# Performance work log

Hardware: AMD Instinct MI355X
Metric: run time of the kernel (lower is better)

## Reference

```python
import jax, jax.numpy as jnp
import numpy as np

SEQ, BATCH, IN = 512, 64, 1024
H, L = 512, 2


def setup_inputs() -> dict:
    key = jax.random.key(0)
    ks = jax.random.split(key, 5)
    s = 0.02
    return {
        "x": jax.random.normal(ks[0], (SEQ, BATCH, IN), dtype=jnp.float32),
        "W_ih": jax.random.normal(ks[1], (L, 2, 4 * H, IN), dtype=jnp.float32) * s,
        "b_ih": jax.random.normal(ks[2], (L, 2, 4 * H), dtype=jnp.float32) * s,
        "W_hh": jax.random.normal(ks[3], (L, 2, 4 * H, H), dtype=jnp.float32) * s,
        "b_hh": jax.random.normal(ks[4], (L, 2, 4 * H), dtype=jnp.float32) * s,
    }


def _run_direction(xs, Wi, bi, Wh, bh, hidden):
    # Precompute the input projection for all timesteps in one big GEMM.
    pre = jnp.einsum("tbd,gd->tbg", xs, Wi) + bi  # [T, B, 4H]

    def step(carry, p):
        h, c = carry
        gates = p + h @ Wh.T + bh
        i, f, g, o = jnp.split(gates, 4, axis=-1)
        # NOTE: faithful to the source module's (nonstandard) gating:
        #   c_t = c_{t-1} * sigmoid(i) + sigmoid(f) * tanh(g)
        c = c * jax.nn.sigmoid(i) + jax.nn.sigmoid(f) * jnp.tanh(g)
        h = jnp.tanh(c) * jax.nn.sigmoid(o)
        return (h, c), h

    B = xs.shape[1]
    h0 = jnp.zeros((B, hidden), xs.dtype)
    c0 = jnp.zeros((B, hidden), xs.dtype)
    _, hs = jax.lax.scan(step, (h0, c0), pre)
    return hs  # [T, B, H]


def reference(x, W_ih, b_ih, W_hh, b_hh):
    hidden = W_hh.shape[-1]
    num_layers = W_ih.shape[0]
    inp = x  # [T, B, D]
    for l in range(num_layers):
        fwd = _run_direction(inp, W_ih[l, 0], b_ih[l, 0], W_hh[l, 0], b_hh[l, 0], hidden)
        bwd = _run_direction(inp[::-1], W_ih[l, 1], b_ih[l, 1], W_hh[l, 1], b_hh[l, 1], hidden)[::-1]
        inp = jnp.concatenate([fwd, bwd], axis=-1)  # [T, B, 2H]
    return inp
```

## Files before the change

kernel.cpp:

```cpp
#include <hip/hip_runtime.h>

#define TSEQ 512
#define BATCH 64
#define DIN 1024
#define HID 512
#define G4 2048
#define CHK 64

typedef __attribute__((ext_vector_type(8))) short short8;
typedef __attribute__((ext_vector_type(4))) float floatx4;

__device__ __forceinline__ floatx4 mfma16(short8 a, short8 b, floatx4 c) {
  return __builtin_amdgcn_mfma_f32_16x16x32_bf16(a, b, c, 0, 0, 0);
}

__device__ __forceinline__ unsigned short f2bf(float f) {
  unsigned int u = __float_as_uint(f);
  unsigned int r = (u + 0x7fffu + ((u >> 16) & 1u)) >> 16;
  return (unsigned short)r;
}

__device__ __forceinline__ float sigm(float x) { return 1.f / (1.f + __expf(-x)); }
__device__ __forceinline__ float tanh_f(float x) {
  float xx = fminf(fmaxf(x, -15.f), 15.f);
  float e = __expf(2.f * xx);
  return (e - 1.f) / (e + 1.f);
}

__device__ __forceinline__ unsigned long long coh_load_q(const unsigned long long* p) {
  return __hip_atomic_load(p, __ATOMIC_RELAXED, __HIP_MEMORY_SCOPE_AGENT);
}
__device__ __forceinline__ void coh_store_u32(unsigned int* p, unsigned int v) {
  __hip_atomic_store(p, v, __ATOMIC_RELAXED, __HIP_MEMORY_SCOPE_AGENT);
}

__global__ void k_convert_x(const float* __restrict__ x, unsigned short* __restrict__ xbf, int n4) {
  int i = blockIdx.x * 256 + threadIdx.x;
  if (i >= n4) return;
  floatx4 v = reinterpret_cast<const floatx4*>(x)[i];
  union { unsigned short us[4]; unsigned long long ull; } pk;
  pk.us[0] = f2bf(v[0]); pk.us[1] = f2bf(v[1]); pk.us[2] = f2bf(v[2]); pk.us[3] = f2bf(v[3]);
  reinterpret_cast<unsigned long long*>(xbf)[i] = pk.ull;
}

__global__ void k_prep_w(const float* __restrict__ W, unsigned short* __restrict__ Wf, int K) {
  int mt = blockIdx.x, kt = blockIdx.y, ld = blockIdx.z;
  int lane = threadIdx.x;
  int i = lane & 15;
  int unit = (mt >> 1) * 8 + (i >> 2) * 2 + (mt & 1);
  int row = (i & 3) * HID + unit;
  int k0 = kt * 32 + (lane >> 4) * 8;
  const float* src = W + (size_t)ld * G4 * K + (size_t)row * K + k0;
  unsigned short* dst = Wf + (size_t)ld * G4 * K + (((size_t)mt * (K / 32) + kt) * 64 + lane) * 8;
  for (int j = 0; j < 8; ++j) dst[j] = f2bf(src[j]);
}

__global__ void k_prep_bias(const float* __restrict__ bih, const float* __restrict__ bhh,
                            float* __restrict__ biasf) {
  int idx = blockIdx.x * 256 + threadIdx.x;
  int ld = idx >> 11;
  int rp = idx & 2047;
  int unit = (rp >> 5) * 8 + ((rp >> 2) & 3) * 2 + ((rp >> 4) & 1);
  int row = (rp & 3) * HID + unit;
  biasf[idx] = bih[ld * G4 + row] + bhh[ld * G4 + row];
}

__global__ void k_zero_bar(unsigned int* bar) {
  if (threadIdx.x < 2) bar[threadIdx.x * 64] = 0;
}

__global__ __launch_bounds__(256, 2) void k_proj(
    const unsigned short* __restrict__ xin,
    const unsigned short* __restrict__ Wf,
    const float* __restrict__ biasf,
    float* __restrict__ pre,
    int t0) {
  const int dir = blockIdx.z;
  const int w = threadIdx.x >> 6;
  const int lane = threadIdx.x & 63;
  const int quad = lane >> 4, col = lane & 15;
  const int tloc = blockIdx.y * 4 + w;
  const int tg = dir ? (TSEQ - 1 - (t0 + tloc)) : (t0 + tloc);
  const unsigned short* Wd = Wf + (size_t)dir * G4 * DIN;
  const unsigned short* xrow = xin + (size_t)tg * BATCH * DIN;

  floatx4 acc[8][4];
#pragma unroll
  for (int mi = 0; mi < 8; ++mi)
#pragma unroll
    for (int ni = 0; ni < 4; ++ni) acc[mi][ni] = (floatx4){0.f, 0.f, 0.f, 0.f};

#pragma unroll 4
  for (int kt = 0; kt < 32; ++kt) {
    short8 bfr[4];
#pragma unroll
    for (int ni = 0; ni < 4; ++ni) {
      int b = ni * 16 + col;
      bfr[ni] = *reinterpret_cast<const short8*>(xrow + (size_t)b * DIN + kt * 32 + quad * 8);
    }
#pragma unroll
    for (int mi = 0; mi < 8; ++mi) {
      size_t mt = (size_t)(blockIdx.x * 8 + mi);
      short8 afr = *reinterpret_cast<const short8*>(Wd + ((mt * 32 + kt) * 64 + lane) * 8);
#pragma unroll
      for (int ni = 0; ni < 4; ++ni) acc[mi][ni] = mfma16(afr, bfr[ni], acc[mi][ni]);
    }
  }

#pragma unroll
  for (int mi = 0; mi < 8; ++mi) {
    int gbase = blockIdx.x * 128 + mi * 16 + quad * 4;
#pragma unroll
    for (int r = 0; r < 4; ++r) {
      float bv = biasf[dir * G4 + gbase + r];
      float* prow = pre + (((size_t)dir * CHK + tloc) * G4 + gbase + r) * BATCH;
#pragma unroll
      for (int ni = 0; ni < 4; ++ni) prow[ni * 16 + col] = acc[mi][ni][r] + bv;
    }
  }
}

__device__ __forceinline__ void dir_barrier(unsigned int* ctr, unsigned int target) {
  __syncthreads();
  if (threadIdx.x == 0) {
    __hip_atomic_fetch_add(ctr, 1u, __ATOMIC_RELAXED, __HIP_MEMORY_SCOPE_AGENT);
    while (__hip_atomic_load(ctr, __ATOMIC_RELAXED, __HIP_MEMORY_SCOPE_AGENT) < target) {
      __builtin_amdgcn_s_sleep(1);
    }
  }
  __syncthreads();
}

__global__ __launch_bounds__(256, 1) void k_steps(
    const unsigned short* __restrict__ Whhf,
    const float* __restrict__ pre,
    unsigned short* act1bf,
    unsigned short* hT2,
    float* cst,
    float* __restrict__ dout,
    unsigned int* bar,
    int t0, int layer, unsigned int bar_base) {
  const int dir = blockIdx.y;
  const int gb = blockIdx.x;
  const int w = threadIdx.x >> 6;
  const int lane = threadIdx.x & 63;
  const int quad = lane >> 4, col = lane & 15;
  const int b = w * 16 + col;
  unsigned int* ctr = bar + dir * 64;

  const unsigned short* Wd = Whhf + (size_t)dir * G4 * HID;
  short8 wfr[16][2];
#pragma unroll
  for (int kt = 0; kt < 16; ++kt)
#pragma unroll
    for (int mi = 0; mi < 2; ++mi) {
      size_t mt = (size_t)(gb * 2 + mi);
      wfr[kt][mi] = *reinterpret_cast<const short8*>(Wd + ((mt * 16 + kt) * 64 + lane) * 8);
    }
#pragma unroll
  for (int kt = 0; kt < 16; ++kt) {
    asm volatile("" : "+v"(wfr[kt][0]), "+v"(wfr[kt][1]));
  }

  float* cl = cst + ((size_t)layer * 2 + dir) * HID * BATCH;
  const int u0 = gb * 8 + quad * 2;
  const int u1 = u0 + 1;
  float c0 = 0.f, c1 = 0.f;
  if (t0 > 0) { c0 = cl[u0 * BATCH + b]; c1 = cl[u1 * BATCH + b]; }

  float pf[2][4];
#pragma unroll
  for (int mi = 0; mi < 2; ++mi)
#pragma unroll
    for (int r = 0; r < 4; ++r) {
      int gp = gb * 32 + mi * 16 + quad * 4 + r;
      pf[mi][r] = pre[(((size_t)dir * CHK + 0) * G4 + gp) * BATCH + b];
    }

  for (int j = 0; j < CHK; ++j) {
    const int s = t0 + j;
    const int t = dir ? (TSEQ - 1 - s) : s;

    floatx4 acc[2];
#pragma unroll
    for (int mi = 0; mi < 2; ++mi)
#pragma unroll
      for (int r = 0; r < 4; ++r) acc[mi][r] = pf[mi][r];

    if (j + 1 < CHK) {
#pragma unroll
      for (int mi = 0; mi < 2; ++mi)
#pragma unroll
        for (int r = 0; r < 4; ++r) {
          int gp = gb * 32 + mi * 16 + quad * 4 + r;
          pf[mi][r] = pre[(((size_t)dir * CHK + (j + 1)) * G4 + gp) * BATCH + b];
        }
    }

    if (s > 0) {
      const unsigned short* hprev;
      int hstride;
      if (layer == 0) {
        int tp = dir ? t + 1 : t - 1;
        hprev = act1bf + (size_t)tp * BATCH * DIN + dir * HID;
        hstride = DIN;
      } else {
        hprev = hT2 + (size_t)(((s - 1) & 1) * 2 + dir) * BATCH * HID;
        hstride = HID;
      }
      const unsigned long long* hq =
          reinterpret_cast<const unsigned long long*>(hprev + (size_t)b * hstride);
      short8 hb[16];
#pragma unroll
      for (int kt = 0; kt < 16; ++kt) {
        union { unsigned long long q[2]; short8 v; } u;
        u.q[0] = coh_load_q(hq + kt * 8 + quad * 2);
        u.q[1] = coh_load_q(hq + kt * 8 + quad * 2 + 1);
        hb[kt] = u.v;
      }
#pragma unroll
      for (int kt = 0; kt < 16; ++kt) {
        acc[0] = mfma16(wfr[kt][0], hb[kt], acc[0]);
        acc[1] = mfma16(wfr[kt][1], hb[kt], acc[1]);
      }
    }

    float si = sigm(acc[0][0]);
    float sf = sigm(acc[0][1]);
    float tg = tanh_f(acc[0][2]);
    float so = sigm(acc[0][3]);
    c0 = c0 * si + sf * tg;
    float h0 = tanh_f(c0) * so;

    si = sigm(acc[1][0]);
    sf = sigm(acc[1][1]);
    tg = tanh_f(acc[1][2]);
    so = sigm(acc[1][3]);
    c1 = c1 * si + sf * tg;
    float h1 = tanh_f(c1) * so;

    unsigned int hp = (unsigned int)f2bf(h0) | ((unsigned int)f2bf(h1) << 16);
    if (layer == 0) {
      unsigned short* arow = act1bf + ((size_t)t * BATCH + b) * DIN + dir * HID;
      coh_store_u32(reinterpret_cast<unsigned int*>(arow + u0), hp);
    } else {
      unsigned short* hrow2 = hT2 + ((size_t)((s & 1) * 2 + dir) * BATCH + b) * HID;
      coh_store_u32(reinterpret_cast<unsigned int*>(hrow2 + u0), hp);
      float* drow = dout + ((size_t)t * BATCH + b) * DIN + dir * HID;
      *reinterpret_cast<float2*>(drow + u0) = make_float2(h0, h1);
    }

    if (j + 1 < CHK) {
      dir_barrier(ctr, bar_base + (unsigned)(j + 1) * 64);
    }
  }

  cl[u0 * BATCH + b] = c0;
  cl[u1 * BATCH + b] = c1;
}

extern "C" void kernel_launch(void* const* d_in, const int* in_sizes, int n_in,
                              void* d_out, int out_size, void* d_ws, size_t ws_size,
                              hipStream_t stream) {
  const float* x = (const float*)d_in[0];
  const float* W_ih = (const float*)d_in[1];
  const float* b_ih = (const float*)d_in[2];
  const float* W_hh = (const float*)d_in[3];
  const float* b_hh = (const float*)d_in[4];
  float* dout = (float*)d_out;

  char* p = (char*)d_ws;
  auto alloc = [&](size_t bytes) {
    char* r = p;
    p += (bytes + 255) & ~(size_t)255;
    return r;
  };
  unsigned short* xbf    = (unsigned short*)alloc((size_t)TSEQ * BATCH * DIN * 2);
  unsigned short* act1bf = (unsigned short*)alloc((size_t)TSEQ * BATCH * DIN * 2);
  float*          pre    = (float*)alloc((size_t)2 * CHK * G4 * BATCH * 4);
  unsigned short* Wihf   = (unsigned short*)alloc((size_t)4 * G4 * DIN * 2);
  unsigned short* Whhf   = (unsigned short*)alloc((size_t)4 * G4 * HID * 2);
  float*          biasf  = (float*)alloc((size_t)4 * G4 * 4);
  float*          cst    = (float*)alloc((size_t)4 * HID * BATCH * 4);
  unsigned short* hT2    = (unsigned short*)alloc((size_t)4 * BATCH * HID * 2);
  unsigned int*   bar    = (unsigned int*)alloc(512);

  size_t required = (size_t)(p - (char*)d_ws);
  if (ws_size < required) return;

  int n4 = TSEQ * BATCH * DIN / 4;
  k_zero_bar<<<dim3(1), dim3(64), 0, stream>>>(bar);
  k_convert_x<<<dim3((n4 + 255) / 256), dim3(256), 0, stream>>>(x, xbf, n4);
  k_prep_w<<<dim3(G4 / 16, DIN / 32, 4), dim3(64), 0, stream>>>(W_ih, Wihf, DIN);
  k_prep_w<<<dim3(G4 / 16, HID / 32, 4), dim3(64), 0, stream>>>(W_hh, Whhf, HID);
  k_prep_bias<<<dim3(32), dim3(256), 0, stream>>>(b_ih, b_hh, biasf);

  unsigned int bar_base = 0;
  for (int l = 0; l < 2; ++l) {
    const unsigned short* xin = l ? act1bf : xbf;
    const unsigned short* Wfl = Wihf + (size_t)l * 2 * G4 * DIN;
    const unsigned short* Whl = Whhf + (size_t)l * 2 * G4 * HID;
    const float* bfl = biasf + (size_t)l * 2 * G4;
    for (int c = 0; c < TSEQ / CHK; ++c) {
      k_proj<<<dim3(G4 / 128, CHK / 4, 2), dim3(256), 0, stream>>>(xin, Wfl, bfl, pre, c * CHK);
      k_steps<<<dim3(G4 / 32, 2), dim3(256), 0, stream>>>(Whl, pre, act1bf, hT2, cst, dout,
                                                          bar, c * CHK, l, bar_base);
      bar_base += (unsigned)(CHK - 1) * 64;
    }
  }
  (void)in_sizes; (void)n_in; (void)out_size;
}
```

Baseline: 7.178 ms.

## Replace atomic-counter grid barrier with per-block flags and stage W_hh in LDS

Each block in the recurrent kernel now publishes its progress to its own padded flag slot instead of incrementing a shared atomic counter. Consumers wait only right before they read the previous hidden state: every wave polls all 64 flags of its direction and uses a wave-wide vote to decide when to proceed. This targets atomic contention and the trailing barrier latency on the serial per-timestep path. Separately, the recurrent weight fragments move from held VGPRs into a 32KB shared-memory tile that is re-read every step. That frees registers but adds LDS read latency to the critical loop.

```diff
diff --git a/kernel.cpp b/kernel.cpp
--- a/kernel.cpp
+++ b/kernel.cpp
@@ -28,6 +28,9 @@
 }
 
 __device__ __forceinline__ unsigned long long coh_load_q(const unsigned long long* p) {
+  return __hip_atomic_load(p, __ATOMIC_RELAXED, __HIP_MEMORY_SCOPE_AGENT);
+}
+__device__ __forceinline__ unsigned int coh_load_u32(const unsigned int* p) {
   return __hip_atomic_load(p, __ATOMIC_RELAXED, __HIP_MEMORY_SCOPE_AGENT);
 }
 __device__ __forceinline__ void coh_store_u32(unsigned int* p, unsigned int v) {
@@ -66,7 +69,8 @@
 }
 
 __global__ void k_zero_bar(unsigned int* bar) {
-  if (threadIdx.x < 2) bar[threadIdx.x * 64] = 0;
+  int i = threadIdx.x;
+  if (i < 128) bar[i * 16] = 0;
 }
 
 __global__ __launch_bounds__(256, 2) void k_proj(
@@ -120,15 +124,14 @@
   }
 }
 
-__device__ __forceinline__ void dir_barrier(unsigned int* ctr, unsigned int target) {
-  __syncthreads();
-  if (threadIdx.x == 0) {
-    __hip_atomic_fetch_add(ctr, 1u, __ATOMIC_RELAXED, __HIP_MEMORY_SCOPE_AGENT);
-    while (__hip_atomic_load(ctr, __ATOMIC_RELAXED, __HIP_MEMORY_SCOPE_AGENT) < target) {
-      __builtin_amdgcn_s_sleep(1);
-    }
-  }
-  __syncthreads();
+__device__ __forceinline__ void wait_flags(const unsigned int* flags, unsigned int target) {
+  const int lane = threadIdx.x & 63;
+  const unsigned int* p = flags + lane * 16;
+  while (true) {
+    unsigned int v = coh_load_u32(p);
+    if (__all((int)(v >= target))) break;
+    __builtin_amdgcn_s_sleep(1);
+  }
 }
 
 __global__ __launch_bounds__(256, 1) void k_steps(
@@ -146,20 +149,15 @@
   const int lane = threadIdx.x & 63;
   const int quad = lane >> 4, col = lane & 15;
   const int b = w * 16 + col;
-  unsigned int* ctr = bar + dir * 64;
-
-  const unsigned short* Wd = Whhf + (size_t)dir * G4 * HID;
-  short8 wfr[16][2];
-#pragma unroll
-  for (int kt = 0; kt < 16; ++kt)
-#pragma unroll
-    for (int mi = 0; mi < 2; ++mi) {
-      size_t mt = (size_t)(gb * 2 + mi);
-      wfr[kt][mi] = *reinterpret_cast<const short8*>(Wd + ((mt * 16 + kt) * 64 + lane) * 8);
-    }
-#pragma unroll
-  for (int kt = 0; kt < 16; ++kt) {
-    asm volatile("" : "+v"(wfr[kt][0]), "+v"(wfr[kt][1]));
+  unsigned int* flags = bar + dir * 1024;
+
+  __shared__ unsigned short wlds[32 * HID];
+  {
+    const uint4* src = reinterpret_cast<const uint4*>(
+        Whhf + (size_t)dir * G4 * HID + (size_t)gb * 16384);
+    uint4* dst = reinterpret_cast<uint4*>(wlds);
+#pragma unroll
+    for (int it = 0; it < 8; ++it) dst[it * 256 + threadIdx.x] = src[it * 256 + threadIdx.x];
   }
 
   float* cl = cst + ((size_t)layer * 2 + dir) * HID * BATCH;
@@ -177,6 +175,8 @@
       pf[mi][r] = pre[(((size_t)dir * CHK + 0) * G4 + gp) * BATCH + b];
     }
 
+  __syncthreads();
+
   for (int j = 0; j < CHK; ++j) {
     const int s = t0 + j;
     const int t = dir ? (TSEQ - 1 - s) : s;
@@ -198,6 +198,8 @@
     }
 
     if (s > 0) {
+      if (j >= 1) wait_flags(flags, bar_base + (unsigned)j);
+
       const unsigned short* hprev;
       int hstride;
       if (layer == 0) {
@@ -220,8 +222,10 @@
       }
 #pragma unroll
       for (int kt = 0; kt < 16; ++kt) {
-        acc[0] = mfma16(wfr[kt][0], hb[kt], acc[0]);
-        acc[1] = mfma16(wfr[kt][1], hb[kt], acc[1]);
+        short8 w0 = *reinterpret_cast<const short8*>(wlds + ((0 * 16 + kt) * 64 + lane) * 8);
+        short8 w1 = *reinterpret_cast<const short8*>(wlds + ((1 * 16 + kt) * 64 + lane) * 8);
+        acc[0] = mfma16(w0, hb[kt], acc[0]);
+        acc[1] = mfma16(w1, hb[kt], acc[1]);
       }
     }
 
@@ -251,7 +255,8 @@
     }
 
     if (j + 1 < CHK) {
-      dir_barrier(ctr, bar_base + (unsigned)(j + 1) * 64);
+      __syncthreads();
+      if (threadIdx.x == 0) coh_store_u32(flags + gb * 16, bar_base + (unsigned)(j + 1));
     }
   }
 
@@ -283,13 +288,13 @@
   float*          biasf  = (float*)alloc((size_t)4 * G4 * 4);
   float*          cst    = (float*)alloc((size_t)4 * HID * BATCH * 4);
   unsigned short* hT2    = (unsigned short*)alloc((size_t)4 * BATCH * HID * 2);
-  unsigned int*   bar    = (unsigned int*)alloc(512);
+  unsigned int*   bar    = (unsigned int*)alloc((size_t)2 * 64 * 16 * 4);
 
   size_t required = (size_t)(p - (char*)d_ws);
   if (ws_size < required) return;
 
   int n4 = TSEQ * BATCH * DIN / 4;
-  k_zero_bar<<<dim3(1), dim3(64), 0, stream>>>(bar);
+  k_zero_bar<<<dim3(1), dim3(128), 0, stream>>>(bar);
   k_convert_x<<<dim3((n4 + 255) / 256), dim3(256), 0, stream>>>(x, xbf, n4);
   k_prep_w<<<dim3(G4 / 16, DIN / 32, 4), dim3(64), 0, stream>>>(W_ih, Wihf, DIN);
   k_prep_w<<<dim3(G4 / 16, HID / 32, 4), dim3(64), 0, stream>>>(W_hh, Whhf, HID);
@@ -305,7 +310,7 @@
       k_proj<<<dim3(G4 / 128, CHK / 4, 2), dim3(256), 0, stream>>>(xin, Wfl, bfl, pre, c * CHK);
       k_steps<<<dim3(G4 / 32, 2), dim3(256), 0, stream>>>(Whl, pre, act1bf, hT2, cst, dout,
                                                           bar, c * CHK, l, bar_base);
-      bar_base += (unsigned)(CHK - 1) * 64;
+      bar_base += (unsigned)(CHK - 1);
     }
   }
   (void)in_sizes; (void)n_in; (void)out_size;
```

Result: faster. 6.490 ms (-9.6%).
